# Performance work log

Measured on AMD Instinct MI355X. Metric: run time of the kernel, lower is better.

Reference implementation:

```python
import jax, jax.numpy as jnp
import numpy as np

E, B, T = 7, 50, 100               # ensemble (network_size), no_batches=50, time blocks
D, A, L, H, C = 128, 32, 256, 1024, 128  # data, action, latent, hidden, context sizes
H_STEP = 0.1                        # (t1 - t0) / T == dt -> one SDE step per block


def setup_inputs() -> dict:
    key = jax.random.key(0)
    ks = iter(jax.random.split(key, 64))
    def nrm(shape, scale=1.0):
        return jax.random.normal(next(ks), shape, jnp.float32) * scale
    def ens(i, o):
        s = 1.0 / np.sqrt(i)
        return nrm((E, i, o), s), nrm((E, o), s)
    def lin(i, o):
        s = 1.0 / np.sqrt(i)
        return nrm((i, o), s), nrm((o,), s)
    inp = {}
    inp["enc_w1"], inp["enc_b1"] = ens(D, H)
    inp["enc_w2"], inp["enc_b2"] = ens(H, H)
    inp["enc_w3"], inp["enc_b3"] = ens(H, C)
    inp["qz0_w"], inp["qz0_b"] = ens(C, 2 * L)
    inp["act_w"], inp["act_b"] = ens(L + A + D, L)
    inp["proj_w1"], inp["proj_b1"] = ens(L, H)
    inp["proj_w2"], inp["proj_b2"] = ens(H, H)
    inp["proj_w3"], inp["proj_b3"] = ens(H, D)
    inp["f_w1"], inp["f_b1"] = lin(L, H)
    inp["f_w2"], inp["f_b2"] = lin(H, H)
    inp["f_w3"], inp["f_b3"] = lin(H, L)
    inp["h_w1"], inp["h_b1"] = lin(L, H)
    inp["h_w2"], inp["h_b2"] = lin(H, H)
    inp["h_w3"], inp["h_b3"] = lin(H, L)
    # per-latent-dim g nets: Linear(1,H) -> ReLU -> Linear(H,1), stacked over L dims
    inp["g_w1"] = nrm((L, H), 0.2)
    inp["g_b1"] = nrm((L, H), 0.2)
    inp["g_w2"] = nrm((L, H), 0.2 / np.sqrt(H))
    inp["g_b2"] = 0.5 + nrm((L,), 0.01)   # keep diffusion bounded away from 0
    inp["pz0_mean"] = jnp.zeros((E, 1, L), jnp.float32)
    inp["pz0_logstd"] = jnp.zeros((E, 1, L), jnp.float32)
    inp["xs"] = nrm((E, T * B, D))
    inp["actions"] = nrm((E, T * B, A))
    inp["eps_z0"] = nrm((T, E, B, L))      # torch.randn_like noise for z0 reparam
    inp["dw_noise"] = nrm((T, E * B, L))   # Brownian increment noise (unit std)
    return inp


def reference(enc_w1, enc_b1, enc_w2, enc_b2, enc_w3, enc_b3,
              qz0_w, qz0_b, act_w, act_b,
              proj_w1, proj_b1, proj_w2, proj_b2, proj_w3, proj_b3,
              f_w1, f_b1, f_w2, f_b2, f_w3, f_b3,
              h_w1, h_b1, h_w2, h_b2, h_w3, h_b3,
              g_w1, g_b1, g_w2, g_b2,
              pz0_mean, pz0_logstd,
              xs, actions, eps_z0, dw_noise):
    def ens_lin(x, w, b):  # EnsembleFC: bmm + bias
        return jnp.einsum('ebi,eio->ebo', x, w) + b[:, None, :]

    def encoder(x):
        x = jax.nn.relu(ens_lin(x, enc_w1, enc_b1))
        x = jax.nn.relu(ens_lin(x, enc_w2, enc_b2))
        return ens_lin(x, enc_w3, enc_b3)

    def projector(z):
        z = jnp.tanh(ens_lin(z, proj_w1, proj_b1))
        z = jnp.tanh(ens_lin(z, proj_w2, proj_b2))
        return ens_lin(z, proj_w3, proj_b3)

    def mlp(y, w1, b1, w2, b2, w3, b3):  # Linear-ReLU-Linear-Tanh-Linear
        y = jax.nn.relu(y @ w1 + b1)
        y = jnp.tanh(y @ w2 + b2)
        return y @ w3 + b3

    def g_fn(y):  # vectorized per-dim tiny MLPs: y (N, L) -> (N, L)
        hh = jax.nn.relu(y[:, :, None] * g_w1[None] + g_b1[None])  # (N, L, H)
        return jnp.sum(hh * g_w2[None], axis=-1) + g_b2

    xs_t = jnp.moveaxis(xs.reshape(E, T, B, D), 1, 0)        # (T, E, B, D)
    act_t = jnp.moveaxis(actions.reshape(E, T, B, A), 1, 0)  # (T, E, B, A)
    sqrt_h = jnp.sqrt(jnp.float32(H_STEP))

    def step(carry, inps):
        zs_last, i = carry
        x_i, a_i, eps_i, dw_i = inps
        ctx = encoder(x_i)                                  # (E, B, C)
        q = ens_lin(ctx, qz0_w, qz0_b)                      # (E, B, 2L)
        qm, ql = q[..., :L], q[..., L:]
        z0 = qm + jnp.exp(ql) * eps_i
        z_in = jnp.where(i == 0, z0, zs_last)               # first step uses z0
        lad = jnp.concatenate([z_in, a_i, x_i], axis=2)
        z = ens_lin(lad, act_w, act_b).reshape(E * B, L)
        # one SDE step with logqp (f: posterior drift, h: prior drift, g: diffusion)
        fv = mlp(z, f_w1, f_b1, f_w2, f_b2, f_w3, f_b3)
        hv = mlp(z, h_w1, h_b1, h_w2, h_b2, h_w3, h_b3)
        gv = g_fn(z)
        u = (fv - hv) / gv
        lr = 0.5 * jnp.sum(u * u, axis=-1) * H_STEP         # (E*B,) log-ratio increment
        z_new = z + fv * H_STEP + gv * (sqrt_h * dw_i)
        zs_new = z_new.reshape(E, B, L)
        xm = projector(zs_new)                              # (E, B, D)
        # KL(q(z0) || p(z0)) for diagonal Gaussians
        kl = (pz0_logstd - ql) \
             + (jnp.exp(2.0 * ql) + (qm - pz0_mean) ** 2) / (2.0 * jnp.exp(2.0 * pz0_logstd)) \
             - 0.5
        logqp0 = kl.sum(axis=2).mean(axis=1)                # (E,)
        lr_mean = lr.reshape(E, B).mean(axis=1)             # (E,)
        return (zs_new, i + 1), (lr_mean, logqp0, xm)

    init = (jnp.zeros((E, B, L), xs.dtype), jnp.int32(0))
    (_, _), (lrm, lq0, xms) = jax.lax.scan(step, init, (xs_t, act_t, eps_z0, dw_noise))
    logqp_path = lrm.sum(axis=0) + lq0.sum(axis=0)          # (E,)
    predicted_xs = jnp.moveaxis(xms, 0, 1).reshape(E, T * B, D)
    return logqp_path, predicted_xs
```

## Files before the change

kernel.cpp:

```cpp
#include <hip/hip_runtime.h>
#include <hip/hip_bf16.h>
#include <math.h>

#define E_ 7
#define B_ 50
#define T_ 100
#define D_ 128
#define A_ 32
#define L_ 256
#define H_ 1024
#define C_ 128
#define EB_ 350
#define TB_ 5000
#define SQRTH 0.31622776601683794f

typedef __attribute__((ext_vector_type(8))) short s8v;
typedef __attribute__((ext_vector_type(4))) float f32x4;
typedef _Float16 f16x2 __attribute__((ext_vector_type(2)));
typedef __hip_bfloat16 bf16;

#define MFMA __builtin_amdgcn_mfma_f32_16x16x32_bf16

__device__ __forceinline__ int lswz(int row, int ck) {
  return ((ck & ~7) | ((ck ^ row) & 7)) << 3;
}

struct BG {
  const bf16* A[8];
  const bf16* W[8];
  const float* bias[8];
  float* Cf[8];
  bf16* Cb[8];
};

template<int BM, int ACT, int OUT>
__global__ __launch_bounds__(256)
void bgemm(BG g, int M, int K, int lda, int ldw, int ldc) {
  __shared__ short As[BM * 64];
  __shared__ short Ws[128 * 64];
  const short* Ap = (const short*)g.A[blockIdx.z];
  const short* Wp = (const short*)g.W[blockIdx.z];
  const int bm = blockIdx.x * BM, bn = blockIdx.y * 128;
  const int tid = threadIdx.x;
  const int wv = tid >> 6, lane = tid & 63;
  const int wm0 = (wv >> 1) * (BM / 2), wn0 = (wv & 1) * 64;
  const int l15 = lane & 15, l4 = lane >> 4;
  constexpr int FM = BM / 32;
  constexpr int AI = BM / 32;
  f32x4 acc[FM][4] = {};
  for (int k0 = 0; k0 < K; k0 += 64) {
    s8v av[AI], wvv[4];
#pragma unroll
    for (int i = 0; i < AI; ++i) {
      const int c = tid + i * 256, r = c >> 3, ck = c & 7;
      s8v v = {};
      if (bm + r < M) v = *(const s8v*)(Ap + (size_t)(bm + r) * lda + k0 + ck * 8);
      av[i] = v;
    }
#pragma unroll
    for (int i = 0; i < 4; ++i) {
      const int c = tid + i * 256, r = c >> 3, ck = c & 7;
      wvv[i] = *(const s8v*)(Wp + (size_t)(bn + r) * ldw + k0 + ck * 8);
    }
    __syncthreads();
#pragma unroll
    for (int i = 0; i < AI; ++i) {
      const int c = tid + i * 256, r = c >> 3, ck = c & 7;
      *(s8v*)(As + r * 64 + ((ck ^ (r & 7)) << 3)) = av[i];
    }
#pragma unroll
    for (int i = 0; i < 4; ++i) {
      const int c = tid + i * 256, r = c >> 3, ck = c & 7;
      *(s8v*)(Ws + r * 64 + ((ck ^ (r & 7)) << 3)) = wvv[i];
    }
    __syncthreads();
#pragma unroll
    for (int ks = 0; ks < 2; ++ks) {
      s8v af[FM], bfr[4];
#pragma unroll
      for (int m = 0; m < FM; ++m) {
        const int r = wm0 + m * 16 + l15, ck = ks * 4 + l4;
        af[m] = *(const s8v*)(As + r * 64 + ((ck ^ (r & 7)) << 3));
      }
#pragma unroll
      for (int n = 0; n < 4; ++n) {
        const int r = wn0 + n * 16 + l15, ck = ks * 4 + l4;
        bfr[n] = *(const s8v*)(Ws + r * 64 + ((ck ^ (r & 7)) << 3));
      }
#pragma unroll
      for (int m = 0; m < FM; ++m)
#pragma unroll
        for (int n = 0; n < 4; ++n)
          acc[m][n] = MFMA(af[m], bfr[n], acc[m][n], 0, 0, 0);
    }
    __syncthreads();
  }
  const float* bias = g.bias[blockIdx.z];
// ... 102 lines not shown
                 const float* __restrict__ gw2, _Float16* __restrict__ dst) {
  const int idx = blockIdx.x * 256 + threadIdx.x;
  if (idx >= 256 * 3 * 1024) return;
  const int l = idx / 3072, rem = idx - l * 3072, arr = rem >> 10, h = rem & 1023;
  const float* s = arr == 0 ? gw1 : (arr == 1 ? gb1 : gw2);
  dst[idx] = (_Float16)s[(size_t)l * 1024 + h];
}

__global__ __launch_bounds__(256)
void qkl_kernel(const float* __restrict__ ctx, int rows, int row_off, int ctx_estride,
                const float* __restrict__ qw, const float* __restrict__ qb,
                const float* __restrict__ pm, const float* __restrict__ pl,
                const float* __restrict__ eps0, bf16* __restrict__ z0hi,
                bf16* __restrict__ z0lo, float* __restrict__ logqp) {
  __shared__ float cx[16][128];
  __shared__ float red[16];
  const int e = blockIdx.y;
  const int r0 = blockIdx.x * 16;
  const int tid = threadIdx.x;
  {
    const int r = tid >> 4, c = (tid & 15) * 8;
    float4 v0 = make_float4(0.f, 0.f, 0.f, 0.f), v1 = v0;
    if (r0 + r < rows) {
      const float* src = ctx + (size_t)e * ctx_estride + (size_t)(r0 + r) * C_ + c;
      v0 = *(const float4*)src;
      v1 = *(const float4*)(src + 4);
    }
    *(float4*)&cx[r][c] = v0;
    *(float4*)&cx[r][c + 4] = v1;
  }
  if (tid < 16) red[tid] = 0.f;
  __syncthreads();
  const int j = tid;
  const float* w = qw + (size_t)e * C_ * 512;
  float am_[16] = {};
  float al_[16] = {};
  for (int k0 = 0; k0 < C_; k0 += 4) {
    float wm[4], wl[4];
#pragma unroll
    for (int q = 0; q < 4; ++q) {
      wm[q] = w[(size_t)(k0 + q) * 512 + j];
      wl[q] = w[(size_t)(k0 + q) * 512 + 256 + j];
    }
#pragma unroll
    for (int r = 0; r < 16; ++r) {
      const float4 cv = *(const float4*)&cx[r][k0];
      const float cc[4] = {cv.x, cv.y, cv.z, cv.w};
#pragma unroll
      for (int q = 0; q < 4; ++q) {
        am_[r] = fmaf(cc[q], wm[q], am_[r]);
        al_[r] = fmaf(cc[q], wl[q], al_[r]);
      }
    }
  }
  const float qbm = qb[(size_t)e * 512 + j];
  const float qbl = qb[(size_t)e * 512 + 256 + j];
  const float pmv = pm[(size_t)e * L_ + j];
  const float plv = pl[(size_t)e * L_ + j];
  const float inv2e = 0.5f * expf(-2.f * plv);
#pragma unroll
  for (int r = 0; r < 16; ++r) {
    float kl = 0.f;
    if (r0 + r < rows) {
      const float qm_ = am_[r] + qbm;
      const float ql_ = al_[r] + qbl;
      const float dm = qm_ - pmv;
      kl = plv - ql_ + (expf(2.f * ql_) + dm * dm) * inv2e - 0.5f;
      const int gi = row_off + r0 + r;
      if (gi < B_) {
        const size_t zi = ((size_t)e * B_ + gi) * L_ + j;
        const float z0 = qm_ + expf(ql_) * eps0[zi];
        const bf16 h = __float2bfloat16(z0);
        z0hi[zi] = h;
        z0lo[zi] = __float2bfloat16(z0 - __bfloat162float(h));
      }
    }
    for (int off = 32; off; off >>= 1) kl += __shfl_xor(kl, off, 64);
    if ((tid & 63) == 0) atomicAdd(&red[r], kl);
  }
  __syncthreads();
  if (tid < 16 && r0 + tid < rows) atomicAdd(&logqp[e], red[tid] * (1.0f / B_));
}

__global__ __launch_bounds__(256, 2)
void k1_act(const bf16* __restrict__ zhi, const bf16* __restrict__ zlo,
            const bf16* __restrict__ wzh, const bf16* __restrict__ wzl,
            const float* __restrict__ axw, float* __restrict__ zP,
            bf16* __restrict__ zPb, int t) {
  __shared__ short Ah[16 * 256];
  __shared__ short Al[16 * 256];
  const int e = blockIdx.z, rb = blockIdx.x, nb = blockIdx.y * 128;
  const int r0 = rb * 13;
  const int nrows = (50 - r0 < 13) ? (50 - r0) : 13;
  const int tid = threadIdx.x, lane = tid & 63, wv = tid >> 6;
  const int l15 = lane & 15, l4 = lane >> 4;
  const short* zh = (const short*)zhi + (size_t)(e * 50 + r0) * 256;
  const short* zl = (const short*)zlo + (size_t)(e * 50 + r0) * 256;
#pragma unroll
  for (int i = 0; i < 2; ++i) {
    const int lin = tid + i * 256, row = lin >> 5, ck = lin & 31;
    s8v vh = {}, vl = {};
    if (row < nrows) {
      vh = *(const s8v*)(zh + row * 256 + ck * 8);
      vl = *(const s8v*)(zl + row * 256 + ck * 8);
    }
    *(s8v*)(Ah + row * 256 + lswz(row, ck)) = vh;
    *(s8v*)(Al + row * 256 + lswz(row, ck)) = vl;
  }
  __syncthreads();
  const short* Bh = (const short*)wzh + (size_t)e * 65536;
  const short* Bl = (const short*)wzl + (size_t)e * 65536;
  f32x4 acc[2] = {};
#pragma unroll
  for (int kt = 0; kt < 8; ++kt) {
    const int ck = kt * 4 + l4;
    const s8v ah = *(const s8v*)(Ah + l15 * 256 + lswz(l15, ck));
    const s8v al = *(const s8v*)(Al + l15 * 256 + lswz(l15, ck));
#pragma unroll
    for (int nt = 0; nt < 2; ++nt) {
      const int ng = nb + wv * 32 + nt * 16;
      const size_t bo = ((size_t)(ng >> 4) * 8 + kt) * 512 + lane * 8;
      const s8v bh = *(const s8v*)(Bh + bo);
      const s8v bl = *(const s8v*)(Bl + bo);
      acc[nt] = MFMA(ah, bh, acc[nt], 0, 0, 0);
      acc[nt] = MFMA(al, bh, acc[nt], 0, 0, 0);
      acc[nt] = MFMA(ah, bl, acc[nt], 0, 0, 0);
    }
  }
#pragma unroll
  for (int nt = 0; nt < 2; ++nt) {
    const int col = nb + wv * 32 + nt * 16 + l15;
#pragma unroll
    for (int j = 0; j < 4; ++j) {
      const int row = l4 * 4 + j;
      if (row < nrows) {
        const int gr = e * 50 + r0 + row;
        const float v = acc[nt][j] + axw[((size_t)e * TB_ + t * 50 + r0 + row) * 256 + col];
        zP[(size_t)gr * 256 + col] = v;
        zPb[(size_t)gr * 256 + col] = __float2bfloat16(v);
      }
    }
  }
}

__global__ __launch_bounds__(256, 2)
void k2_l1(const bf16* __restrict__ zPb, const bf16* __restrict__ w1f,
           const float* __restrict__ fb1, const float* __restrict__ hb1,
           bf16* __restrict__ fh1) {
  __shared__ short As[16 * 256];
  const int rb = blockIdx.x, nb = blockIdx.y * 128;
  const int r0 = rb * 16;
  const int tid = threadIdx.x, lane = tid & 63, wv = tid >> 6;
  const int l15 = lane & 15, l4 = lane >> 4;
#pragma unroll
  for (int i = 0; i < 2; ++i) {
    const int lin = tid + i * 256, row = lin >> 5, ck = lin & 31;
    s8v v = {};
    if (r0 + row < EB_)
      v = *(const s8v*)((const short*)zPb + (size_t)(r0 + row) * 256 + ck * 8);
    *(s8v*)(As + row * 256 + lswz(row, ck)) = v;
  }
  __syncthreads();
  f32x4 acc[2] = {};
#pragma unroll
  for (int kt = 0; kt < 8; ++kt) {
    const int ck = kt * 4 + l4;
    const s8v a = *(const s8v*)(As + l15 * 256 + lswz(l15, ck));
#pragma unroll
    for (int nt = 0; nt < 2; ++nt) {
      const int ng = nb + wv * 32 + nt * 16;
      const s8v b = *(const s8v*)((const short*)w1f + ((size_t)(ng >> 4) * 8 + kt) * 512 + lane * 8);
      acc[nt] = MFMA(a, b, acc[nt], 0, 0, 0);
    }
  }
#pragma unroll
  for (int nt = 0; nt < 2; ++nt) {
    const int col = nb + wv * 32 + nt * 16 + l15;
    const float bv = (col < 1024) ? fb1[col] : hb1[col - 1024];
#pragma unroll
    for (int j = 0; j < 4; ++j) {
      const int row = r0 + l4 * 4 + j;
      if (row < EB_)
        fh1[(size_t)row * 2048 + col] = __float2bfloat16(fmaxf(acc[nt][j] + bv, 0.f));
    }
  }
}

__global__ __launch_bounds__(256, 2)
void k3_l2(const bf16* __restrict__ fh1, const bf16* __restrict__ w2f,
           const float* __restrict__ fb2, const float* __restrict__ hb2,
           bf16* __restrict__ fh2) {
  __shared__ short As[16 * 1024];
  const int rb = blockIdx.x, nbl = blockIdx.y;
  const int nb = nbl * 128, r0 = rb * 16;
  const int half = (nbl >= 8) ? 1024 : 0;
  const int tid = threadIdx.x, lane = tid & 63, wv = tid >> 6;
  const int l15 = lane & 15, l4 = lane >> 4;
#pragma unroll
  for (int i = 0; i < 8; ++i) {
    const int lin = tid + i * 256, row = lin >> 7, ck = lin & 127;
    s8v v = {};
    if (r0 + row < EB_)
      v = *(const s8v*)((const short*)fh1 + (size_t)(r0 + row) * 2048 + half + ck * 8);
    *(s8v*)(As + row * 1024 + lswz(row, ck)) = v;
  }
  __syncthreads();
  f32x4 acc[2] = {};
#pragma unroll 4
  for (int kt = 0; kt < 32; ++kt) {
    const int ck = kt * 4 + l4;
    const s8v a = *(const s8v*)(As + l15 * 1024 + lswz(l15, ck));
#pragma unroll
    for (int nt = 0; nt < 2; ++nt) {
      const int ng = nb + wv * 32 + nt * 16;
      const s8v b = *(const s8v*)((const short*)w2f + ((size_t)(ng >> 4) * 32 + kt) * 512 + lane * 8);
      acc[nt] = MFMA(a, b, acc[nt], 0, 0, 0);
    }
  }
#pragma unroll
  for (int nt = 0; nt < 2; ++nt) {
    const int col = nb + wv * 32 + nt * 16 + l15;
    const float bv = half ? hb2[col - 1024] : fb2[col];
#pragma unroll
    for (int j = 0; j < 4; ++j) {
      const int row = r0 + l4 * 4 + j;
      if (row < EB_)
        fh2[(size_t)row * 2048 + col] = __float2bfloat16(tanhf(acc[nt][j] + bv));
    }
  }
}

__global__ __launch_bounds__(256, 1)
void k4_fin(const bf16* __restrict__ fh2, const bf16* __restrict__ w3f,
            const float* __restrict__ fb3, const float* __restrict__ hb3,
            const _Float16* __restrict__ gpk, const float* __restrict__ gb2,
            const float* __restrict__ zP, const float* __restrict__ dw,
            bf16* __restrict__ zhi, bf16* __restrict__ zlo,
            bf16* __restrict__ zs_bf, float* __restrict__ logqp, int t) {
  __shared__ short As[16 * 1024];
  __shared__ float ztile[16][64];
  __shared__ float gvt[16][64];
  __shared__ float ebuck[8];
  const int rb = blockIdx.x, cb = blockIdx.y;
  const int r0 = rb * 16, c0 = cb * 64;
  const int tid = threadIdx.x, lane = tid & 63, wv = tid >> 6;
  const int l15 = lane & 15, l4 = lane >> 4;
  if (tid < 8) ebuck[tid] = 0.f;
#pragma unroll
  for (int i = 0; i < 4; ++i) {
    const int lin = tid + i * 256, row = lin >> 6, col = lin & 63;
    ztile[row][col] = (r0 + row < EB_) ? zP[(size_t)(r0 + row) * 256 + c0 + col] : 1.0f;
  }
  f32x4 accF = {}, accH = {};
#pragma unroll
  for (int fb = 0; fb < 2; ++fb) {
    __syncthreads();
#pragma unroll
    for (int i = 0; i < 8; ++i) {
      const int lin = tid + i * 256, row = lin >> 7, ck = lin & 127;
      s8v v = {};
      if (r0 + row < EB_)
        v = *(const s8v*)((const short*)fh2 + (size_t)(r0 + row) * 2048 + fb * 1024 + ck * 8);
      *(s8v*)(As + row * 1024 + lswz(row, ck)) = v;
    }
    __syncthreads();
    const int ng = fb * 256 + c0 + wv * 16;
    f32x4 acc = {};
#pragma unroll 4
    for (int kt = 0; kt < 32; ++kt) {
      const int ck = kt * 4 + l4;
      const s8v a = *(const s8v*)(As + l15 * 1024 + lswz(l15, ck));
      const s8v b = *(const s8v*)((const short*)w3f + ((size_t)(ng >> 4) * 32 + kt) * 512 + lane * 8);
      acc = MFMA(a, b, acc, 0, 0, 0);
    }
    if (fb) accH = acc; else accF = acc;
  }
  __syncthreads();
  {
    const int lloc = tid >> 2, hq = tid & 3;
    const _Float16* gl = gpk + (size_t)(c0 + lloc) * 3072 + hq * 256;
    f16x2 z2[16];
#pragma unroll
    for (int r = 0; r < 16; ++r) {
      const _Float16 zh_ = (_Float16)ztile[r][lloc];
      z2[r] = f16x2{zh_, zh_};
    }
    float ga[16] = {};
    for (int hp = 0; hp < 128; ++hp) {
      const f16x2 w1v = *(const f16x2*)(gl + 2 * hp);
      const f16x2 b1v = *(const f16x2*)(gl + 1024 + 2 * hp);
      const f16x2 w2v = *(const f16x2*)(gl + 2048 + 2 * hp);
#pragma unroll
      for (int r = 0; r < 16; ++r) {
        f16x2 tt = z2[r] * w1v + b1v;
#if __has_builtin(__builtin_elementwise_max)
        const f16x2 zz = {};
        tt = __builtin_elementwise_max(tt, zz);
#else
        tt[0] = tt[0] > (_Float16)0 ? tt[0] : (_Float16)0;
        tt[1] = tt[1] > (_Float16)0 ? tt[1] : (_Float16)0;
#endif
#if __has_builtin(__builtin_amdgcn_fdot2)
        ga[r] = __builtin_amdgcn_fdot2(tt, w2v, ga[r], false);
#else
        ga[r] += (float)tt[0] * (float)w2v[0] + (float)tt[1] * (float)w2v[1];
#endif
      }
    }
#pragma unroll
    for (int r = 0; r < 16; ++r) {
      float v = ga[r];
      v += __shfl_xor(v, 1, 64);
      v += __shfl_xor(v, 2, 64);
      if (hq == 0) gvt[r][lloc] = v + gb2[c0 + lloc];
    }
  }
  __syncthreads();
  const int col_loc = wv * 16 + l15, col = c0 + col_loc;
  const float fb3v = fb3[col], hb3v = hb3[col];
#pragma unroll
  for (int j = 0; j < 4; ++j) {
    const int rl = l4 * 4 + j, row = r0 + rl;
    if (row < EB_) {
      const float fv = accF[j] + fb3v;
      const float hv = accH[j] + hb3v;
      const float gv = gvt[rl][col_loc];
      const float u = (fv - hv) / gv;
      atomicAdd(&ebuck[row / 50], 0.001f * u * u);
      const float znew = ztile[rl][col_loc] + 0.1f * fv +
                         gv * (SQRTH * dw[(size_t)t * (EB_ * 256) + (size_t)row * 256 + col]);
      const bf16 h = __float2bfloat16(znew);
      const size_t zi = (size_t)row * 256 + col;
      zhi[zi] = h;
      zlo[zi] = __float2bfloat16(znew - __bfloat162float(h));
      const int e = row / 50, b = row - e * 50;
      zs_bf[((size_t)e * TB_ + t * 50 + b) * 256 + col] = h;
    }
  }
  __syncthreads();
  if (tid < 7) {
    const float v = ebuck[tid];
    if (v != 0.f) atomicAdd(&logqp[tid], v);
  }
}

__global__ void init_kernel(float* logqp) {
  if (threadIdx.x < E_) logqp[threadIdx.x] = 0.f;
}

extern "C" void kernel_launch(void* const* d_in, const int* in_sizes, int n_in,
                              void* d_out, int out_size, void* d_ws, size_t ws_size,
                              hipStream_t stream) {
  (void)in_sizes; (void)n_in; (void)out_size;
  const float* enc_w1 = (const float*)d_in[0];
  const float* enc_b1 = (const float*)d_in[1];
  const float* enc_w2 = (const float*)d_in[2];
  const float* enc_b2 = (const float*)d_in[3];
  const float* enc_w3 = (const float*)d_in[4];
  const float* enc_b3 = (const float*)d_in[5];
  const float* qz0_w  = (const float*)d_in[6];
  const float* qz0_b  = (const float*)d_in[7];
  const float* act_w  = (const float*)d_in[8];
  const float* act_b  = (const float*)d_in[9];
  const float* proj_w1 = (const float*)d_in[10];
  const float* proj_b1 = (const float*)d_in[11];
  const float* proj_w2 = (const float*)d_in[12];
  const float* proj_b2 = (const float*)d_in[13];
  const float* proj_w3 = (const float*)d_in[14];
  const float* proj_b3 = (const float*)d_in[15];
  const float* f_w1 = (const float*)d_in[16];
  const float* f_b1 = (const float*)d_in[17];
  const float* f_w2 = (const float*)d_in[18];
  const float* f_b2 = (const float*)d_in[19];
  const float* f_w3 = (const float*)d_in[20];
  const float* f_b3 = (const float*)d_in[21];
  const float* h_w1 = (const float*)d_in[22];
  const float* h_b1 = (const float*)d_in[23];
  const float* h_w2 = (const float*)d_in[24];
  const float* h_b2 = (const float*)d_in[25];
  const float* h_w3 = (const float*)d_in[26];
  const float* h_b3 = (const float*)d_in[27];
  const float* g_w1 = (const float*)d_in[28];
  const float* g_b1 = (const float*)d_in[29];
  const float* g_w2 = (const float*)d_in[30];
  const float* g_b2 = (const float*)d_in[31];
  const float* pz0_mean   = (const float*)d_in[32];
  const float* pz0_logstd = (const float*)d_in[33];
  const float* xs      = (const float*)d_in[34];
  const float* actions = (const float*)d_in[35];
  const float* eps_z0  = (const float*)d_in[36];
  const float* dw      = (const float*)d_in[37];

  float* out = (float*)d_out;
  float* logqp = out;
  float* pred = out + E_;

  char* base = (char*)d_ws;
  size_t off = 0;
  auto alloc = [&](size_t bytes) {
    void* p = base + off;
    off = (off + bytes + 255) & ~(size_t)255;
    return p;
  };
  bf16* zhi    = (bf16*)alloc((size_t)EB_ * 256 * 2);
  bf16* zlo    = (bf16*)alloc((size_t)EB_ * 256 * 2);
  float* zP    = (float*)alloc((size_t)EB_ * 256 * 4);
  bf16* zPb    = (bf16*)alloc((size_t)EB_ * 256 * 2);
  bf16* fh1    = (bf16*)alloc((size_t)EB_ * 2048 * 2);
  bf16* fh2    = (bf16*)alloc((size_t)EB_ * 2048 * 2);
  bf16* zs_bf  = (bf16*)alloc((size_t)E_ * T_ * B_ * 256 * 2);
  float* axw   = (float*)alloc((size_t)E_ * TB_ * 256 * 4);
  bf16* ax_bf  = (bf16*)alloc((size_t)E_ * TB_ * 192 * 2);
  bf16* waxT   = (bf16*)alloc((size_t)E_ * 256 * 192 * 2);
  bf16* wzh    = (bf16*)alloc((size_t)E_ * 65536 * 2);
  bf16* wzl    = (bf16*)alloc((size_t)E_ * 65536 * 2);
  bf16* w1f    = (bf16*)alloc((size_t)2048 * 256 * 2);
  bf16* w2f    = (bf16*)alloc((size_t)2048 * 1024 * 2);
  bf16* w3f    = (bf16*)alloc((size_t)512 * 1024 * 2);
  _Float16* gpk = (_Float16*)alloc((size_t)256 * 3 * 1024 * 2);
  bf16* xs_bf  = (bf16*)alloc((size_t)E_ * TB_ * D_ * 2);
  bf16* ew1T = (bf16*)alloc((size_t)E_ * D_ * H_ * 2);
  bf16* ew2T = (bf16*)alloc((size_t)E_ * H_ * H_ * 2);
  bf16* ew3T = (bf16*)alloc((size_t)E_ * H_ * C_ * 2);
  bf16* pw1T = (bf16*)alloc((size_t)E_ * L_ * H_ * 2);
  bf16* pw2T = (bf16*)alloc((size_t)E_ * H_ * H_ * 2);
  bf16* pw3T = (bf16*)alloc((size_t)E_ * H_ * D_ * 2);
  const size_t per_row = (size_t)E_ * (H_ * 2 * 2 + C_ * 4);
  size_t remain = (ws_size > off + 4096) ? (ws_size - off - 4096) : 0;
  int CH = (int)(remain / per_row);
  if (CH > 2500) CH = 2500;
  if (CH < 64) CH = 64;
  bf16* bufA = (bf16*)alloc((size_t)E_ * CH * H_ * 2);
  bf16* bufB = (bf16*)alloc((size_t)E_ * CH * H_ * 2);
  float* bufC = (float*)alloc((size_t)E_ * CH * C_ * 4);

  init_kernel<<<dim3(1), dim3(64), 0, stream>>>(logqp);

  const dim3 cb256(256);
  cvt_kernel<<<dim3((E_ * TB_ * D_ / 4 + 255) / 256), cb256, 0, stream>>>(xs, xs_bf, E_ * TB_ * D_ / 4);
  cvtT_kernel<<<dim3(H_ / 32, D_ / 32, E_), cb256, 0, stream>>>(enc_w1, ew1T, D_, H_, (long)D_ * H_, (long)D_ * H_);
  cvtT_kernel<<<dim3(H_ / 32, H_ / 32, E_), cb256, 0, stream>>>(enc_w2, ew2T, H_, H_, (long)H_ * H_, (long)H_ * H_);
  cvtT_kernel<<<dim3(C_ / 32, H_ / 32, E_), cb256, 0, stream>>>(enc_w3, ew3T, H_, C_, (long)H_ * C_, (long)H_ * C_);
  cvtT_kernel<<<dim3(H_ / 32, L_ / 32, E_), cb256, 0, stream>>>(proj_w1, pw1T, L_, H_, (long)L_ * H_, (long)L_ * H_);
  cvtT_kernel<<<dim3(H_ / 32, H_ / 32, E_), cb256, 0, stream>>>(proj_w2, pw2T, H_, H_, (long)H_ * H_, (long)H_ * H_);
  cvtT_kernel<<<dim3(D_ / 32, H_ / 32, E_), cb256, 0, stream>>>(proj_w3, pw3T, H_, D_, (long)H_ * D_, (long)H_ * D_);
  ax_build<<<dim3((E_ * TB_ * 192 + 255) / 256), cb256, 0, stream>>>(actions, xs, ax_bf);
  waxT_build<<<dim3((E_ * 256 * 192 + 255) / 256), cb256, 0, stream>>>(act_w, waxT);
  packWz<<<dim3((E_ * 65536 + 255) / 256), cb256, 0, stream>>>(act_w, wzh, wzl);
  packW<<<dim3((256 * 1024 + 255) / 256), cb256, 0, stream>>>(f_w1, w1f, 256, 1024);
  packW<<<dim3((256 * 1024 + 255) / 256), cb256, 0, stream>>>(h_w1, w1f + (size_t)1024 * 256, 256, 1024);
  packW<<<dim3((1024 * 1024 + 255) / 256), cb256, 0, stream>>>(f_w2, w2f, 1024, 1024);
  packW<<<dim3((1024 * 1024 + 255) / 256), cb256, 0, stream>>>(h_w2, w2f + (size_t)1024 * 1024, 1024, 1024);
  packW<<<dim3((1024 * 256 + 255) / 256), cb256, 0, stream>>>(f_w3, w3f, 1024, 256);
  packW<<<dim3((1024 * 256 + 255) / 256), cb256, 0, stream>>>(h_w3, w3f + (size_t)256 * 1024, 1024, 256);
  gpack_build<<<dim3((256 * 3 * 1024 + 255) / 256), cb256, 0, stream>>>(g_w1, g_b1, g_w2, gpk);

  BG g;
  for (int e = 0; e < E_; ++e) {
    g.A[e] = ax_bf + (size_t)e * TB_ * 192;
    g.W[e] = waxT + (size_t)e * 256 * 192;
    g.bias[e] = act_b + (size_t)e * 256;
    g.Cf[e] = axw + (size_t)e * TB_ * 256;
  }
  bgemm<128, 0, 0><<<dim3((TB_ + 127) / 128, 2, E_), 256, 0, stream>>>(g, TB_, 192, 192, 192, 256);

  for (int c = 0; c < TB_; c += CH) {
    const int rows = (TB_ - c < CH) ? (TB_ - c) : CH;
    const int mt = (rows + 127) / 128;
    for (int e = 0; e < E_; ++e) {
      g.A[e] = xs_bf + ((size_t)e * TB_ + c) * D_;
      g.W[e] = ew1T + (size_t)e * D_ * H_;
      g.bias[e] = enc_b1 + (size_t)e * H_;
      g.Cb[e] = bufA + (size_t)e * CH * H_;
    }
    bgemm<128, 1, 1><<<dim3(mt, H_ / 128, E_), 256, 0, stream>>>(g, rows, D_, D_, D_, H_);
    for (int e = 0; e < E_; ++e) {
      g.A[e] = bufA + (size_t)e * CH * H_;
      g.W[e] = ew2T + (size_t)e * H_ * H_;
      g.bias[e] = enc_b2 + (size_t)e * H_;
      g.Cb[e] = bufB + (size_t)e * CH * H_;
    }
    bgemm<128, 1, 1><<<dim3(mt, H_ / 128, E_), 256, 0, stream>>>(g, rows, H_, H_, H_, H_);
    for (int e = 0; e < E_; ++e) {
      g.A[e] = bufB + (size_t)e * CH * H_;
      g.W[e] = ew3T + (size_t)e * H_ * C_;
      g.bias[e] = enc_b3 + (size_t)e * C_;
      g.Cf[e] = bufC + (size_t)e * CH * C_;
    }
    bgemm<128, 0, 0><<<dim3(mt, C_ / 128, E_), 256, 0, stream>>>(g, rows, H_, H_, H_, C_);
    qkl_kernel<<<dim3((rows + 15) / 16, E_), 256, 0, stream>>>(
        bufC, rows, c, CH * C_, qz0_w, qz0_b, pz0_mean, pz0_logstd, eps_z0,
        zhi, zlo, logqp);
  }

  for (int t = 0; t < T_; ++t) {
    k1_act<<<dim3(4, 2, E_), 256, 0, stream>>>(zhi, zlo, wzh, wzl, axw, zP, zPb, t);
    k2_l1<<<dim3(22, 16), 256, 0, stream>>>(zPb, w1f, f_b1, h_b1, fh1);
    k3_l2<<<dim3(22, 16), 256, 0, stream>>>(fh1, w2f, f_b2, h_b2, fh2);
    k4_fin<<<dim3(22, 4), 256, 0, stream>>>(fh2, w3f, f_b3, h_b3, gpk, g_b2,
                                            zP, dw, zhi, zlo, zs_bf, logqp, t);
  }

  for (int c = 0; c < TB_; c += CH) {
    const int rows = (TB_ - c < CH) ? (TB_ - c) : CH;
    const int mt = (rows + 127) / 128;
    for (int e = 0; e < E_; ++e) {
      g.A[e] = zs_bf + ((size_t)e * T_ * B_ + c) * L_;
      g.W[e] = pw1T + (size_t)e * L_ * H_;
      g.bias[e] = proj_b1 + (size_t)e * H_;
      g.Cb[e] = bufA + (size_t)e * CH * H_;
    }
    bgemm<128, 2, 1><<<dim3(mt, H_ / 128, E_), 256, 0, stream>>>(g, rows, L_, L_, L_, H_);
    for (int e = 0; e < E_; ++e) {
      g.A[e] = bufA + (size_t)e * CH * H_;
      g.W[e] = pw2T + (size_t)e * H_ * H_;
      g.bias[e] = proj_b2 + (size_t)e * H_;
      g.Cb[e] = bufB + (size_t)e * CH * H_;
    }
    bgemm<128, 2, 1><<<dim3(mt, H_ / 128, E_), 256, 0, stream>>>(g, rows, H_, H_, H_, H_);
    for (int e = 0; e < E_; ++e) {
      g.A[e] = bufB + (size_t)e * CH * H_;
      g.W[e] = pw3T + (size_t)e * H_ * D_;
      g.bias[e] = proj_b3 + (size_t)e * D_;
      g.Cf[e] = pred + ((size_t)e * TB_ + c) * D_;
    }
    bgemm<128, 0, 0><<<dim3(mt, D_ / 128, E_), 256, 0, stream>>>(g, rows, H_, H_, H_, D_);
  }
}
```

Measured before the change: 10.30 ms.

## Fuse per-timestep SDE kernels into one persistent cooperative kernel with grid barriers

Replaces the four kernel launches per time step (400 launches) with a single persistent cooperative kernel of 256 workgroups. Stages are separated by a hierarchical atomic grid barrier. The diffusion g-net evaluation moves off the final stage and runs on idle workgroups during the L1/L2 stages, and the L1/L2 tiles are widened to 256 columns. The log-ratio sums are now accumulated in registers and reduced once at the end. The aim is to remove launch overhead and overlap the g computation. The cost is barrier latency, a relaxed-atomic barrier that must be correct, and the assumption that all 256 workgroups are co-resident.

```diff
diff --git a/kernel.cpp b/kernel.cpp
--- a/kernel.cpp
+++ b/kernel.cpp
@@ -13,6 +13,7 @@
 #define EB_ 350
 #define TB_ 5000
 #define SQRTH 0.31622776601683794f
+#define NWG 256
 
 typedef __attribute__((ext_vector_type(8))) short s8v;
 typedef __attribute__((ext_vector_type(4))) float f32x4;
@@ -281,270 +282,312 @@
   if (tid < 16 && r0 + tid < rows) atomicAdd(&logqp[e], red[tid] * (1.0f / B_));
 }
 
-__global__ __launch_bounds__(256, 2)
-void k1_act(const bf16* __restrict__ zhi, const bf16* __restrict__ zlo,
-            const bf16* __restrict__ wzh, const bf16* __restrict__ wzl,
-            const float* __restrict__ axw, float* __restrict__ zP,
-            bf16* __restrict__ zPb, int t) {
-  __shared__ short Ah[16 * 256];
-  __shared__ short Al[16 * 256];
-  const int e = blockIdx.z, rb = blockIdx.x, nb = blockIdx.y * 128;
-  const int r0 = rb * 13;
-  const int nrows = (50 - r0 < 13) ? (50 - r0) : 13;
-  const int tid = threadIdx.x, lane = tid & 63, wv = tid >> 6;
-  const int l15 = lane & 15, l4 = lane >> 4;
-  const short* zh = (const short*)zhi + (size_t)(e * 50 + r0) * 256;
-  const short* zl = (const short*)zlo + (size_t)(e * 50 + r0) * 256;
-#pragma unroll
-  for (int i = 0; i < 2; ++i) {
-    const int lin = tid + i * 256, row = lin >> 5, ck = lin & 31;
-    s8v vh = {}, vl = {};
-    if (row < nrows) {
-      vh = *(const s8v*)(zh + row * 256 + ck * 8);
-      vl = *(const s8v*)(zl + row * 256 + ck * 8);
-    }
-    *(s8v*)(Ah + row * 256 + lswz(row, ck)) = vh;
-    *(s8v*)(Al + row * 256 + lswz(row, ck)) = vl;
-  }
+struct SK {
+  const bf16 *wzh, *wzl, *w1f, *w2f, *w3f;
+  const _Float16* gpk;
+  const float *fb1, *hb1, *fb2, *hb2, *fb3, *hb3, *gb2;
+  const float *axw, *dw;
+  float *zP, *gv;
+  bf16 *zPb, *fh1, *fh2, *zhi, *zlo, *zs_bf;
+  float* logqp;
+  unsigned* bar;
+};
+
+__device__ __forceinline__ void gsync(unsigned* bar, unsigned ph, int tid, int wg,
+                                      int* sRel) {
+  __threadfence();
   __syncthreads();
-  const short* Bh = (const short*)wzh + (size_t)e * 65536;
-  const short* Bl = (const short*)wzl + (size_t)e * 65536;
-  f32x4 acc[2] = {};
-#pragma unroll
-  for (int kt = 0; kt < 8; ++kt) {
-    const int ck = kt * 4 + l4;
-    const s8v ah = *(const s8v*)(Ah + l15 * 256 + lswz(l15, ck));
-    const s8v al = *(const s8v*)(Al + l15 * 256 + lswz(l15, ck));
-#pragma unroll
-    for (int nt = 0; nt < 2; ++nt) {
-      const int ng = nb + wv * 32 + nt * 16;
-      const size_t bo = ((size_t)(ng >> 4) * 8 + kt) * 512 + lane * 8;
-      const s8v bh = *(const s8v*)(Bh + bo);
-      const s8v bl = *(const s8v*)(Bl + bo);
-      acc[nt] = MFMA(ah, bh, acc[nt], 0, 0, 0);
-      acc[nt] = MFMA(al, bh, acc[nt], 0, 0, 0);
-      acc[nt] = MFMA(ah, bl, acc[nt], 0, 0, 0);
-    }
-  }
-#pragma unroll
-  for (int nt = 0; nt < 2; ++nt) {
-    const int col = nb + wv * 32 + nt * 16 + l15;
-#pragma unroll
-    for (int j = 0; j < 4; ++j) {
-      const int row = l4 * 4 + j;
-      if (row < nrows) {
-        const int gr = e * 50 + r0 + row;
-        const float v = acc[nt][j] + axw[((size_t)e * TB_ + t * 50 + r0 + row) * 256 + col];
-        zP[(size_t)gr * 256 + col] = v;
-        zPb[(size_t)gr * 256 + col] = __float2bfloat16(v);
-      }
-    }
-  }
-}
-
-__global__ __launch_bounds__(256, 2)
-void k2_l1(const bf16* __restrict__ zPb, const bf16* __restrict__ w1f,
-           const float* __restrict__ fb1, const float* __restrict__ hb1,
-           bf16* __restrict__ fh1) {
-  __shared__ short As[16 * 256];
-  const int rb = blockIdx.x, nb = blockIdx.y * 128;
-  const int r0 = rb * 16;
-  const int tid = threadIdx.x, lane = tid & 63, wv = tid >> 6;
-  const int l15 = lane & 15, l4 = lane >> 4;
-#pragma unroll
-  for (int i = 0; i < 2; ++i) {
-    const int lin = tid + i * 256, row = lin >> 5, ck = lin & 31;
-    s8v v = {};
-    if (r0 + row < EB_)
-      v = *(const s8v*)((const short*)zPb + (size_t)(r0 + row) * 256 + ck * 8);
-    *(s8v*)(As + row * 256 + lswz(row, ck)) = v;
+  if (tid == 0) {
+    *sRel = 0;
+    const unsigned v = __hip_atomic_fetch_add(&bar[(wg >> 4) * 32], 1u,
+                                              __ATOMIC_RELAXED, __HIP_MEMORY_SCOPE_AGENT);
+    if (v + 1u == ph * 16u) {
+      const unsigned r = __hip_atomic_fetch_add(&bar[512], 1u,
+                                                __ATOMIC_RELAXED, __HIP_MEMORY_SCOPE_AGENT);
+      if (r + 1u == ph * 16u) *sRel = 1;
+    }
   }
   __syncthreads();
-  f32x4 acc[2] = {};
-#pragma unroll
-  for (int kt = 0; kt < 8; ++kt) {
-    const int ck = kt * 4 + l4;
-    const s8v a = *(const s8v*)(As + l15 * 256 + lswz(l15, ck));
-#pragma unroll
-    for (int nt = 0; nt < 2; ++nt) {
-      const int ng = nb + wv * 32 + nt * 16;
-      const s8v b = *(const s8v*)((const short*)w1f + ((size_t)(ng >> 4) * 8 + kt) * 512 + lane * 8);
-      acc[nt] = MFMA(a, b, acc[nt], 0, 0, 0);
-    }
-  }
-#pragma unroll
-  for (int nt = 0; nt < 2; ++nt) {
-    const int col = nb + wv * 32 + nt * 16 + l15;
-    const float bv = (col < 1024) ? fb1[col] : hb1[col - 1024];
-#pragma unroll
-    for (int j = 0; j < 4; ++j) {
-      const int row = r0 + l4 * 4 + j;
-      if (row < EB_)
-        fh1[(size_t)row * 2048 + col] = __float2bfloat16(fmaxf(acc[nt][j] + bv, 0.f));
-    }
-  }
-}
-
-__global__ __launch_bounds__(256, 2)
-void k3_l2(const bf16* __restrict__ fh1, const bf16* __restrict__ w2f,
-           const float* __restrict__ fb2, const float* __restrict__ hb2,
-           bf16* __restrict__ fh2) {
-  __shared__ short As[16 * 1024];
-  const int rb = blockIdx.x, nbl = blockIdx.y;
-  const int nb = nbl * 128, r0 = rb * 16;
-  const int half = (nbl >= 8) ? 1024 : 0;
-  const int tid = threadIdx.x, lane = tid & 63, wv = tid >> 6;
-  const int l15 = lane & 15, l4 = lane >> 4;
-#pragma unroll
-  for (int i = 0; i < 8; ++i) {
-    const int lin = tid + i * 256, row = lin >> 7, ck = lin & 127;
-    s8v v = {};
-    if (r0 + row < EB_)
-      v = *(const s8v*)((const short*)fh1 + (size_t)(r0 + row) * 2048 + half + ck * 8);
-    *(s8v*)(As + row * 1024 + lswz(row, ck)) = v;
+  if (*sRel)
+    __hip_atomic_store(&bar[544 + tid * 32], ph, __ATOMIC_RELAXED, __HIP_MEMORY_SCOPE_AGENT);
+  if (tid == 0) {
+    while (__hip_atomic_load(&bar[544 + wg * 32], __ATOMIC_RELAXED,
+                             __HIP_MEMORY_SCOPE_AGENT) < ph)
+      __builtin_amdgcn_s_sleep(8);
   }
   __syncthreads();
-  f32x4 acc[2] = {};
-#pragma unroll 4
-  for (int kt = 0; kt < 32; ++kt) {
-    const int ck = kt * 4 + l4;
-    const s8v a = *(const s8v*)(As + l15 * 1024 + lswz(l15, ck));
-#pragma unroll
-    for (int nt = 0; nt < 2; ++nt) {
-      const int ng = nb + wv * 32 + nt * 16;
-      const s8v b = *(const s8v*)((const short*)w2f + ((size_t)(ng >> 4) * 32 + kt) * 512 + lane * 8);
-      acc[nt] = MFMA(a, b, acc[nt], 0, 0, 0);
-    }
-  }
-#pragma unroll
-  for (int nt = 0; nt < 2; ++nt) {
-    const int col = nb + wv * 32 + nt * 16 + l15;
-    const float bv = half ? hb2[col - 1024] : fb2[col];
-#pragma unroll
-    for (int j = 0; j < 4; ++j) {
-      const int row = r0 + l4 * 4 + j;
-      if (row < EB_)
-        fh2[(size_t)row * 2048 + col] = __float2bfloat16(tanhf(acc[nt][j] + bv));
-    }
-  }
-}
-
-__global__ __launch_bounds__(256, 1)
-void k4_fin(const bf16* __restrict__ fh2, const bf16* __restrict__ w3f,
-            const float* __restrict__ fb3, const float* __restrict__ hb3,
-            const _Float16* __restrict__ gpk, const float* __restrict__ gb2,
-            const float* __restrict__ zP, const float* __restrict__ dw,
-            bf16* __restrict__ zhi, bf16* __restrict__ zlo,
-            bf16* __restrict__ zs_bf, float* __restrict__ logqp, int t) {
-  __shared__ short As[16 * 1024];
-  __shared__ float ztile[16][64];
-  __shared__ float gvt[16][64];
-  __shared__ float ebuck[8];
-  const int rb = blockIdx.x, cb = blockIdx.y;
+  __threadfence();
+}
+
+__device__ void g_tile(const SK& a, int gt, int tid) {
+  const int rb = gt >> 2, cb = gt & 3;
   const int r0 = rb * 16, c0 = cb * 64;
-  const int tid = threadIdx.x, lane = tid & 63, wv = tid >> 6;
-  const int l15 = lane & 15, l4 = lane >> 4;
-  if (tid < 8) ebuck[tid] = 0.f;
-#pragma unroll
-  for (int i = 0; i < 4; ++i) {
-    const int lin = tid + i * 256, row = lin >> 6, col = lin & 63;
-    ztile[row][col] = (r0 + row < EB_) ? zP[(size_t)(r0 + row) * 256 + c0 + col] : 1.0f;
-  }
-  f32x4 accF = {}, accH = {};
-#pragma unroll
-  for (int fb = 0; fb < 2; ++fb) {
-    __syncthreads();
-#pragma unroll
-    for (int i = 0; i < 8; ++i) {
-      const int lin = tid + i * 256, row = lin >> 7, ck = lin & 127;
-      s8v v = {};
-      if (r0 + row < EB_)
-        v = *(const s8v*)((const short*)fh2 + (size_t)(r0 + row) * 2048 + fb * 1024 + ck * 8);
-      *(s8v*)(As + row * 1024 + lswz(row, ck)) = v;
-    }
-    __syncthreads();
-    const int ng = fb * 256 + c0 + wv * 16;
-    f32x4 acc = {};
-#pragma unroll 4
-    for (int kt = 0; kt < 32; ++kt) {
-      const int ck = kt * 4 + l4;
-      const s8v a = *(const s8v*)(As + l15 * 1024 + lswz(l15, ck));
-      const s8v b = *(const s8v*)((const short*)w3f + ((size_t)(ng >> 4) * 32 + kt) * 512 + lane * 8);
-      acc = MFMA(a, b, acc, 0, 0, 0);
-    }
-    if (fb) accH = acc; else accF = acc;
-  }
-  __syncthreads();
-  {
-    const int lloc = tid >> 2, hq = tid & 3;
-    const _Float16* gl = gpk + (size_t)(c0 + lloc) * 3072 + hq * 256;
-    f16x2 z2[16];
+  const int lloc = tid >> 2, hq = tid & 3;
+  const _Float16* gl = a.gpk + (size_t)(c0 + lloc) * 3072 + hq * 256;
+  f16x2 z2[16];
+#pragma unroll
+  for (int r = 0; r < 16; ++r) {
+    const float zf = (r0 + r < EB_) ? a.zP[(size_t)(r0 + r) * 256 + c0 + lloc] : 0.f;
+    const _Float16 zh_ = (_Float16)zf;
+    z2[r] = f16x2{zh_, zh_};
+  }
+  float ga[16] = {};
+  for (int hp = 0; hp < 128; ++hp) {
+    const f16x2 w1v = *(const f16x2*)(gl + 2 * hp);
+    const f16x2 b1v = *(const f16x2*)(gl + 1024 + 2 * hp);
+    const f16x2 w2v = *(const f16x2*)(gl + 2048 + 2 * hp);
 #pragma unroll
     for (int r = 0; r < 16; ++r) {
-      const _Float16 zh_ = (_Float16)ztile[r][lloc];
-      z2[r] = f16x2{zh_, zh_};
-    }
-    float ga[16] = {};
-    for (int hp = 0; hp < 128; ++hp) {
-      const f16x2 w1v = *(const f16x2*)(gl + 2 * hp);
-      const f16x2 b1v = *(const f16x2*)(gl + 1024 + 2 * hp);
-      const f16x2 w2v = *(const f16x2*)(gl + 2048 + 2 * hp);
-#pragma unroll
-      for (int r = 0; r < 16; ++r) {
-        f16x2 tt = z2[r] * w1v + b1v;
+      f16x2 tt = z2[r] * w1v + b1v;
 #if __has_builtin(__builtin_elementwise_max)
-        const f16x2 zz = {};
-        tt = __builtin_elementwise_max(tt, zz);
+      const f16x2 zz = {};
+      tt = __builtin_elementwise_max(tt, zz);
 #else
-        tt[0] = tt[0] > (_Float16)0 ? tt[0] : (_Float16)0;
-        tt[1] = tt[1] > (_Float16)0 ? tt[1] : (_Float16)0;
+      tt[0] = tt[0] > (_Float16)0 ? tt[0] : (_Float16)0;
+      tt[1] = tt[1] > (_Float16)0 ? tt[1] : (_Float16)0;
 #endif
 #if __has_builtin(__builtin_amdgcn_fdot2)
-        ga[r] = __builtin_amdgcn_fdot2(tt, w2v, ga[r], false);
+      ga[r] = __builtin_amdgcn_fdot2(tt, w2v, ga[r], false);
 #else
-        ga[r] += (float)tt[0] * (float)w2v[0] + (float)tt[1] * (float)w2v[1];
+      ga[r] += (float)tt[0] * (float)w2v[0] + (float)tt[1] * (float)w2v[1];
 #endif
-      }
-    }
-#pragma unroll
-    for (int r = 0; r < 16; ++r) {
-      float v = ga[r];
-      v += __shfl_xor(v, 1, 64);
-      v += __shfl_xor(v, 2, 64);
-      if (hq == 0) gvt[r][lloc] = v + gb2[c0 + lloc];
-    }
-  }
-  __syncthreads();
-  const int col_loc = wv * 16 + l15, col = c0 + col_loc;
-  const float fb3v = fb3[col], hb3v = hb3[col];
-#pragma unroll
-  for (int j = 0; j < 4; ++j) {
-    const int rl = l4 * 4 + j, row = r0 + rl;
-    if (row < EB_) {
-      const float fv = accF[j] + fb3v;
-      const float hv = accH[j] + hb3v;
-      const float gv = gvt[rl][col_loc];
-      const float u = (fv - hv) / gv;
-      atomicAdd(&ebuck[row / 50], 0.001f * u * u);
-      const float znew = ztile[rl][col_loc] + 0.1f * fv +
-                         gv * (SQRTH * dw[(size_t)t * (EB_ * 256) + (size_t)row * 256 + col]);
-      const bf16 h = __float2bfloat16(znew);
-      const size_t zi = (size_t)row * 256 + col;
-      zhi[zi] = h;
-      zlo[zi] = __float2bfloat16(znew - __bfloat162float(h));
-      const int e = row / 50, b = row - e * 50;
-      zs_bf[((size_t)e * TB_ + t * 50 + b) * 256 + col] = h;
-    }
-  }
-  __syncthreads();
-  if (tid < 7) {
-    const float v = ebuck[tid];
-    if (v != 0.f) atomicAdd(&logqp[tid], v);
-  }
-}
-
-__global__ void init_kernel(float* logqp) {
-  if (threadIdx.x < E_) logqp[threadIdx.x] = 0.f;
+    }
+  }
+#pragma unroll
+  for (int r = 0; r < 16; ++r) {
+    float v = ga[r];
+    v += __shfl_xor(v, 1, 64);
+    v += __shfl_xor(v, 2, 64);
+    if (hq == 0 && r0 + r < EB_)
+      a.gv[(size_t)(r0 + r) * 256 + c0 + lloc] = v + a.gb2[c0 + lloc];
+  }
+}
+
+__global__ __launch_bounds__(256, 1) void scan_kernel(SK a) {
+  __shared__ __align__(16) short As[16 * 1024];
+  __shared__ float ztile[16][64];
+  __shared__ int sRel;
+  const int wg = blockIdx.x, tid = threadIdx.x;
+  const int lane = tid & 63, wv = tid >> 6, l15 = lane & 15, l4 = lane >> 4;
+  const int rb4 = wg >> 2, c04 = (wg & 3) * 64, r04 = rb4 * 16;
+  const int e40 = r04 / 50, e41 = (r04 + 15) / 50;
+  float lr0 = 0.f, lr1 = 0.f;
+  unsigned ph = 0;
+
+  for (int t = 0; t < T_; ++t) {
+    if (wg < 56) {
+      short* Ah = As;
+      short* Al = As + 4096;
+      const int e = wg >> 3, sub = wg & 7, rb = sub >> 1, nb = (sub & 1) * 128;
+      const int r0 = rb * 13;
+      const int nrows = (50 - r0 < 13) ? (50 - r0) : 13;
+      const short* zh = (const short*)a.zhi + (size_t)(e * 50 + r0) * 256;
+      const short* zl = (const short*)a.zlo + (size_t)(e * 50 + r0) * 256;
+#pragma unroll
+      for (int i = 0; i < 2; ++i) {
+        const int lin = tid + i * 256, row = lin >> 5, ck = lin & 31;
+        s8v vh = {}, vl = {};
+        if (row < nrows) {
+          vh = *(const s8v*)(zh + row * 256 + ck * 8);
+          vl = *(const s8v*)(zl + row * 256 + ck * 8);
+        }
+        *(s8v*)(Ah + row * 256 + lswz(row, ck)) = vh;
+        *(s8v*)(Al + row * 256 + lswz(row, ck)) = vl;
+      }
+      __syncthreads();
+      const short* Bh = (const short*)a.wzh + (size_t)e * 65536;
+      const short* Bl = (const short*)a.wzl + (size_t)e * 65536;
+      f32x4 acc[2] = {};
+#pragma unroll
+      for (int kt = 0; kt < 8; ++kt) {
+        const int ck = kt * 4 + l4;
+        const s8v ah = *(const s8v*)(Ah + l15 * 256 + lswz(l15, ck));
+        const s8v al = *(const s8v*)(Al + l15 * 256 + lswz(l15, ck));
+#pragma unroll
+        for (int nt = 0; nt < 2; ++nt) {
+          const int ng = nb + wv * 32 + nt * 16;
+          const size_t bo = ((size_t)(ng >> 4) * 8 + kt) * 512 + lane * 8;
+          const s8v bh = *(const s8v*)(Bh + bo);
+          const s8v bl = *(const s8v*)(Bl + bo);
+          acc[nt] = MFMA(ah, bh, acc[nt], 0, 0, 0);
+          acc[nt] = MFMA(al, bh, acc[nt], 0, 0, 0);
+          acc[nt] = MFMA(ah, bl, acc[nt], 0, 0, 0);
+        }
+      }
+#pragma unroll
+      for (int nt = 0; nt < 2; ++nt) {
+        const int col = nb + wv * 32 + nt * 16 + l15;
+#pragma unroll
+        for (int j = 0; j < 4; ++j) {
+          const int row = l4 * 4 + j;
+          if (row < nrows) {
+            const int gr = e * 50 + r0 + row;
+            const float v = acc[nt][j] +
+                a.axw[((size_t)e * TB_ + t * 50 + r0 + row) * 256 + col];
+            a.zP[(size_t)gr * 256 + col] = v;
+            a.zPb[(size_t)gr * 256 + col] = __float2bfloat16(v);
+          }
+        }
+      }
+    }
+    gsync(a.bar, ++ph, tid, wg, &sRel);
+
+    if (wg < 176) {
+      const int rb = wg >> 3, nb = (wg & 7) * 256, r0 = rb * 16;
+#pragma unroll
+      for (int i = 0; i < 2; ++i) {
+        const int lin = tid + i * 256, row = lin >> 5, ck = lin & 31;
+        s8v v = {};
+        if (r0 + row < EB_)
+          v = *(const s8v*)((const short*)a.zPb + (size_t)(r0 + row) * 256 + ck * 8);
+        *(s8v*)(As + row * 256 + lswz(row, ck)) = v;
+      }
+      __syncthreads();
+      f32x4 acc[4] = {};
+#pragma unroll
+      for (int kt = 0; kt < 8; ++kt) {
+        const int ck = kt * 4 + l4;
+        const s8v av = *(const s8v*)(As + l15 * 256 + lswz(l15, ck));
+#pragma unroll
+        for (int nt = 0; nt < 4; ++nt) {
+          const int ng = nb + wv * 64 + nt * 16;
+          const s8v b = *(const s8v*)((const short*)a.w1f +
+                                      ((size_t)(ng >> 4) * 8 + kt) * 512 + lane * 8);
+          acc[nt] = MFMA(av, b, acc[nt], 0, 0, 0);
+        }
+      }
+#pragma unroll
+      for (int nt = 0; nt < 4; ++nt) {
+        const int col = nb + wv * 64 + nt * 16 + l15;
+        const float bv = (col < 1024) ? a.fb1[col] : a.hb1[col - 1024];
+#pragma unroll
+        for (int j = 0; j < 4; ++j) {
+          const int row = r0 + l4 * 4 + j;
+          if (row < EB_)
+            a.fh1[(size_t)row * 2048 + col] = __float2bfloat16(fmaxf(acc[nt][j] + bv, 0.f));
+        }
+      }
+    } else {
+      const int gt = wg - 176;
+      if (gt < 80) g_tile(a, gt, tid);
+    }
+    gsync(a.bar, ++ph, tid, wg, &sRel);
+
+    if (wg < 176) {
+      const int rb = wg >> 3, nbl = wg & 7, nb = nbl * 256, r0 = rb * 16;
+      const int half = (nbl >= 4) ? 1024 : 0;
+#pragma unroll
+      for (int i = 0; i < 8; ++i) {
+        const int lin = tid + i * 256, row = lin >> 7, ck = lin & 127;
+        s8v v = {};
+        if (r0 + row < EB_)
+          v = *(const s8v*)((const short*)a.fh1 + (size_t)(r0 + row) * 2048 + half + ck * 8);
+        *(s8v*)(As + row * 1024 + lswz(row, ck)) = v;
+      }
+      __syncthreads();
+      f32x4 acc[4] = {};
+#pragma unroll 4
+      for (int kt = 0; kt < 32; ++kt) {
+        const int ck = kt * 4 + l4;
+        const s8v av = *(const s8v*)(As + l15 * 1024 + lswz(l15, ck));
+#pragma unroll
+        for (int nt = 0; nt < 4; ++nt) {
+          const int ng = nb + wv * 64 + nt * 16;
+          const s8v b = *(const s8v*)((const short*)a.w2f +
+                                      ((size_t)(ng >> 4) * 32 + kt) * 512 + lane * 8);
+          acc[nt] = MFMA(av, b, acc[nt], 0, 0, 0);
+        }
+      }
+#pragma unroll
+      for (int nt = 0; nt < 4; ++nt) {
+        const int col = nb + wv * 64 + nt * 16 + l15;
+        const float bv = half ? a.hb2[col - 1024] : a.fb2[col];
+#pragma unroll
+        for (int j = 0; j < 4; ++j) {
+          const int row = r0 + l4 * 4 + j;
+          if (row < EB_)
+            a.fh2[(size_t)row * 2048 + col] = __float2bfloat16(tanhf(acc[nt][j] + bv));
+        }
+      }
+    } else {
+      const int gt = 80 + (wg - 176);
+      if (gt < 88) g_tile(a, gt, tid);
+    }
+    gsync(a.bar, ++ph, tid, wg, &sRel);
+
+    if (wg < 88) {
+#pragma unroll
+      for (int i = 0; i < 4; ++i) {
+        const int lin = tid + i * 256, row = lin >> 6, col = lin & 63;
+        ztile[row][col] = (r04 + row < EB_) ? a.zP[(size_t)(r04 + row) * 256 + c04 + col] : 1.0f;
+      }
+      f32x4 accF = {}, accH = {};
+#pragma unroll
+      for (int fb = 0; fb < 2; ++fb) {
+        __syncthreads();
+#pragma unroll
+        for (int i = 0; i < 8; ++i) {
+          const int lin = tid + i * 256, row = lin >> 7, ck = lin & 127;
+          s8v v = {};
+          if (r04 + row < EB_)
+            v = *(const s8v*)((const short*)a.fh2 + (size_t)(r04 + row) * 2048 + fb * 1024 + ck * 8);
+          *(s8v*)(As + row * 1024 + lswz(row, ck)) = v;
+        }
+        __syncthreads();
+        const int ng = fb * 256 + c04 + wv * 16;
+        f32x4 acc = {};
+#pragma unroll 4
+        for (int kt = 0; kt < 32; ++kt) {
+          const int ck = kt * 4 + l4;
+          const s8v av = *(const s8v*)(As + l15 * 1024 + lswz(l15, ck));
+          const s8v b = *(const s8v*)((const short*)a.w3f +
+                                      ((size_t)(ng >> 4) * 32 + kt) * 512 + lane * 8);
+          acc = MFMA(av, b, acc, 0, 0, 0);
+        }
+        if (fb) accH = acc; else accF = acc;
+      }
+      const int col = c04 + wv * 16 + l15;
+      const float fb3v = a.fb3[col], hb3v = a.hb3[col];
+#pragma unroll
+      for (int j = 0; j < 4; ++j) {
+        const int rl = l4 * 4 + j, row = r04 + rl;
+        if (row < EB_) {
+          const float fv = accF[j] + fb3v;
+          const float hv = accH[j] + hb3v;
+          const float gvv = a.gv[(size_t)row * 256 + col];
+          const float u = (fv - hv) / gvv;
+          if (row / 50 == e40) lr0 += u * u; else lr1 += u * u;
+          const float znew = ztile[rl][wv * 16 + l15] + 0.1f * fv +
+              gvv * (SQRTH * a.dw[(size_t)t * (EB_ * 256) + (size_t)row * 256 + col]);
+          const bf16 h = __float2bfloat16(znew);
+          const size_t zi = (size_t)row * 256 + col;
+          a.zhi[zi] = h;
+          a.zlo[zi] = __float2bfloat16(znew - __bfloat162float(h));
+          const int e = row / 50, b = row - e * 50;
+          a.zs_bf[((size_t)e * TB_ + t * 50 + b) * 256 + col] = h;
+        }
+      }
+    }
+    gsync(a.bar, ++ph, tid, wg, &sRel);
+  }
+
+  if (wg < 88) {
+#pragma unroll
+    for (int o = 32; o; o >>= 1) {
+      lr0 += __shfl_xor(lr0, o, 64);
+      lr1 += __shfl_xor(lr1, o, 64);
+    }
+    if (lane == 0) {
+      atomicAdd(&a.logqp[e40], 0.001f * lr0);
+      if (e41 != e40 && e41 < E_) atomicAdd(&a.logqp[e41], 0.001f * lr1);
+    }
+  }
+}
+
+__global__ void init_kernel(float* logqp, unsigned* bar) {
+  const int i = threadIdx.x;
+  if (i < E_) logqp[i] = 0.f;
+  for (int j = i; j < 8736; j += 256) bar[j] = 0u;
 }
 
 extern "C" void kernel_launch(void* const* d_in, const int* in_sizes, int n_in,
@@ -607,6 +650,7 @@
   bf16* zPb    = (bf16*)alloc((size_t)EB_ * 256 * 2);
   bf16* fh1    = (bf16*)alloc((size_t)EB_ * 2048 * 2);
   bf16* fh2    = (bf16*)alloc((size_t)EB_ * 2048 * 2);
+  float* gvb   = (float*)alloc((size_t)EB_ * 256 * 4);
   bf16* zs_bf  = (bf16*)alloc((size_t)E_ * T_ * B_ * 256 * 2);
   float* axw   = (float*)alloc((size_t)E_ * TB_ * 256 * 4);
   bf16* ax_bf  = (bf16*)alloc((size_t)E_ * TB_ * 192 * 2);
@@ -617,6 +661,7 @@
   bf16* w2f    = (bf16*)alloc((size_t)2048 * 1024 * 2);
   bf16* w3f    = (bf16*)alloc((size_t)512 * 1024 * 2);
   _Float16* gpk = (_Float16*)alloc((size_t)256 * 3 * 1024 * 2);
+  unsigned* bar = (unsigned*)alloc(8736 * 4);
   bf16* xs_bf  = (bf16*)alloc((size_t)E_ * TB_ * D_ * 2);
   bf16* ew1T = (bf16*)alloc((size_t)E_ * D_ * H_ * 2);
   bf16* ew2T = (bf16*)alloc((size_t)E_ * H_ * H_ * 2);
@@ -633,7 +678,7 @@
   bf16* bufB = (bf16*)alloc((size_t)E_ * CH * H_ * 2);
   float* bufC = (float*)alloc((size_t)E_ * CH * C_ * 4);
 
-  init_kernel<<<dim3(1), dim3(64), 0, stream>>>(logqp);
+  init_kernel<<<dim3(1), dim3(256), 0, stream>>>(logqp, bar);
 
   const dim3 cb256(256);
   cvt_kernel<<<dim3((E_ * TB_ * D_ / 4 + 255) / 256), cb256, 0, stream>>>(xs, xs_bf, E_ * TB_ * D_ / 4);
@@ -692,12 +737,18 @@
         zhi, zlo, logqp);
   }
 
-  for (int t = 0; t < T_; ++t) {
-    k1_act<<<dim3(4, 2, E_), 256, 0, stream>>>(zhi, zlo, wzh, wzl, axw, zP, zPb, t);
-    k2_l1<<<dim3(22, 16), 256, 0, stream>>>(zPb, w1f, f_b1, h_b1, fh1);
-    k3_l2<<<dim3(22, 16), 256, 0, stream>>>(fh1, w2f, f_b2, h_b2, fh2);
-    k4_fin<<<dim3(22, 4), 256, 0, stream>>>(fh2, w3f, f_b3, h_b3, gpk, g_b2,
-                                            zP, dw, zhi, zlo, zs_bf, logqp, t);
+  SK sk;
+  sk.wzh = wzh; sk.wzl = wzl; sk.w1f = w1f; sk.w2f = w2f; sk.w3f = w3f;
+  sk.gpk = gpk;
+  sk.fb1 = f_b1; sk.hb1 = h_b1; sk.fb2 = f_b2; sk.hb2 = h_b2;
+  sk.fb3 = f_b3; sk.hb3 = h_b3; sk.gb2 = g_b2;
+  sk.axw = axw; sk.dw = dw;
+  sk.zP = zP; sk.gv = gvb; sk.zPb = zPb; sk.fh1 = fh1; sk.fh2 = fh2;
+  sk.zhi = zhi; sk.zlo = zlo; sk.zs_bf = zs_bf; sk.logqp = logqp; sk.bar = bar;
+  void* params[] = {(void*)&sk};
+  if (hipLaunchCooperativeKernel((const void*)scan_kernel, dim3(NWG), dim3(256),
+                                 params, 0, stream) != hipSuccess) {
+    scan_kernel<<<dim3(NWG), dim3(256), 0, stream>>>(sk);
   }
 
   for (int c = 0; c < TB_; c += CH) {
```

Measured after the change: 28.08 ms. 173% more time.
